# Performance work log

Hardware: AMD Instinct MI355X
Metric: run time of the kernel (lower is better)

Reference implementation:

```python
import jax, jax.numpy as jnp
import numpy as np

BLOCK = 16
H = 16
KV = 4
HPG = H // KV
DH = 64
SCALE = 1.0 / np.sqrt(DH).astype(np.float32)


def setup_inputs() -> dict:
    key = jax.random.key(0)
    ks = jax.random.split(key, 7)
    B, Ldec, Lenc, D = 2, 8192, 4096, 1024
    s = 1.0 / np.sqrt(D).astype(np.float32)
    return {
        "hidden_states": jax.random.normal(ks[0], (B, Ldec, D), jnp.float32),
        "encoder_hidden_states": jax.random.normal(ks[1], (B, Lenc, D), jnp.float32),
        "attention_mask": jax.random.randint(ks[2], (B, Lenc), 0, 2, jnp.int32),
        "Wq": jax.random.normal(ks[3], (D, H * DH), jnp.float32) * s,
        "Wk": jax.random.normal(ks[4], (D, KV * DH), jnp.float32) * s,
        "Wv": jax.random.normal(ks[5], (D, KV * DH), jnp.float32) * s,
        "Wo": jax.random.normal(ks[6], (H * DH, D), jnp.float32) * s,
    }


def reference(hidden_states, encoder_hidden_states, attention_mask, Wq, Wk, Wv, Wo):
    B, Ldec, D = hidden_states.shape
    Lenc = encoder_hidden_states.shape[1]
    pad = (BLOCK - Ldec % BLOCK) % BLOCK
    x = jnp.pad(hidden_states, ((0, 0), (0, pad), (0, 0))) if pad else hidden_states
    nb = (Ldec + pad) // BLOCK
    # mean-pool decoder tokens into blocks: [B, nb, D]
    pooled = x.reshape(B, nb, BLOCK, D).mean(axis=2)
    # projections; GQA: group q heads by kv head (repeat_interleave order)
    q = (pooled @ Wq).reshape(B, nb, KV, HPG, DH)          # [B, nb, KV, HPG, DH]
    k = (encoder_hidden_states @ Wk).reshape(B, Lenc, KV, DH)
    v = (encoder_hidden_states @ Wv).reshape(B, Lenc, KV, DH)
    scores = jnp.einsum("bngqd,blgd->bgqnl", q, k) * SCALE  # [B, KV, HPG, nb, Lenc]
    mask = (attention_mask == 0)[:, None, None, None, :]
    scores = jnp.where(mask, jnp.float32(-1e9), scores)
    attn = jax.nn.softmax(scores, axis=-1)
    out = jnp.einsum("bgqnl,blgd->bngqd", attn, v)          # [B, nb, KV, HPG, DH]
    out = out.reshape(B, nb, H * DH) @ Wo                   # [B, nb, D]
    # broadcast block output back to token level
    unpooled = jnp.broadcast_to(out[:, :, None, :], (B, nb, BLOCK, D)).reshape(B, nb * BLOCK, D)
    return unpooled[:, :Ldec, :]
```

## Files before the change

### kernel.cpp

```cpp
#include <hip/hip_runtime.h>


typedef unsigned short u16;
typedef __attribute__((ext_vector_type(8))) __bf16 bf16x8;
typedef __attribute__((ext_vector_type(4))) float f32x4;
typedef __attribute__((ext_vector_type(4))) _Float16 f16x4;

static __device__ __forceinline__ u16 f2bf(float f) {
    unsigned int u = __float_as_uint(f);
    u = (u + 0x7fffu + ((u >> 16) & 1u)) >> 16;
    return (u16)u;
}
static __device__ __forceinline__ void gload16(const u16* g, u16* l) {
    __builtin_amdgcn_global_load_lds(
        (const __attribute__((address_space(1))) void*)g,
        (__attribute__((address_space(3))) void*)l, 16, 0, 0);
}

__global__ __launch_bounds__(256) void prep_all(const float* __restrict__ enc,
                                                const float* __restrict__ hid,
                                                const int* __restrict__ mask,
                                                const float* __restrict__ Wq,
                                                const float* __restrict__ Wk,
                                                const float* __restrict__ Wv,
                                                const float* __restrict__ Wo,
                                                u16* __restrict__ encb,
                                                u16* __restrict__ poolb,
                                                u16* __restrict__ mh,
                                                u16* __restrict__ Wq_t,
                                                u16* __restrict__ Wkv_t,
                                                u16* __restrict__ Wo_t) {
    int bid = blockIdx.x;
    if (bid < 1024) {
        const int row = bid;
        const int c4 = threadIdx.x;
        const float4* src = (const float4*)(hid + (size_t)row * 16 * 1024) + c4;
        float4 v[16];
#pragma unroll
        for (int t = 0; t < 16; ++t) v[t] = src[(size_t)t * 256];
#pragma unroll
        for (int t = 0; t < 8; ++t) {
            v[t].x += v[t + 8].x; v[t].y += v[t + 8].y;
            v[t].z += v[t + 8].z; v[t].w += v[t + 8].w;
        }
#pragma unroll
        for (int t = 0; t < 4; ++t) {
            v[t].x += v[t + 4].x; v[t].y += v[t + 4].y;
            v[t].z += v[t + 4].z; v[t].w += v[t + 4].w;
        }
#pragma unroll
        for (int t = 0; t < 2; ++t) {
            v[t].x += v[t + 2].x; v[t].y += v[t + 2].y;
            v[t].z += v[t + 2].z; v[t].w += v[t + 2].w;
        }
        v[0].x += v[1].x; v[0].y += v[1].y; v[0].z += v[1].z; v[0].w += v[1].w;
        ushort4 o;
        o.x = f2bf(v[0].x * 0.0625f); o.y = f2bf(v[0].y * 0.0625f);
        o.z = f2bf(v[0].z * 0.0625f); o.w = f2bf(v[0].w * 0.0625f);
        *(ushort4*)(poolb + (size_t)row * 1024 + c4 * 4) = o;
    } else if (bid < 2048) {
        const int base = (bid - 1024) * 2048 + threadIdx.x;
        float4 v[8];
#pragma unroll
        for (int j = 0; j < 8; ++j) v[j] = ((const float4*)enc)[base + j * 256];
#pragma unroll
        for (int j = 0; j < 8; ++j) {
            ushort4 o;
            o.x = f2bf(v[j].x); o.y = f2bf(v[j].y);
            o.z = f2bf(v[j].z); o.w = f2bf(v[j].w);
            ((ushort4*)encb)[base + j * 256] = o;
        }
    } else if (bid < 4608) {
        bid -= 2048;
        const float* in; u16* out; int N, nbx, rowoff;
        if (bid < 1024)      { in = Wq; out = Wq_t;  N = 1024; nbx = 32; rowoff = 0; }
        else if (bid < 2048) { in = Wo; out = Wo_t;  N = 1024; nbx = 32; rowoff = 0; bid -= 1024; }
        else if (bid < 2304) { in = Wk; out = Wkv_t; N = 256;  nbx = 8;  rowoff = 0; bid -= 2048; }
        else                 { in = Wv; out = Wkv_t; N = 256;  nbx = 8;  rowoff = 256; bid -= 2304; }
        const int n0 = (bid % nbx) * 32, k0 = (bid / nbx) * 32;
        __shared__ float t[32][33];
        const int tx = threadIdx.x & 31, ty = threadIdx.x >> 5;
#pragma unroll
        for (int i = 0; i < 4; ++i)
            t[ty + 8 * i][tx] = in[(size_t)(k0 + ty + 8 * i) * N + n0 + tx];
        __syncthreads();
#pragma unroll
        for (int i = 0; i < 4; ++i)
            out[(size_t)(rowoff + n0 + ty + 8 * i) * 1024 + k0 + tx] = f2bf(t[tx][ty + 8 * i]);
    } else {
#pragma unroll
        for (int k = 0; k < 32; ++k) {
            const int i = threadIdx.x + 256 * k;
            mh[i] = mask[i] ? (u16)0x3C00 : (u16)0;
        }
    }
}

template <int MODE>
static __device__ __forceinline__ void gemm_core(const u16* __restrict__ A,
                                                 const u16* __restrict__ Bt,
                                                 u16* __restrict__ outQ,
                                                 float* __restrict__ out_f,
                                                 int m0, int n0, int kt0, int nkt,
                                                 u16* sAB) {
    u16* sA = sAB;
    u16* sB = sAB + 64 * 64;
    const int t = threadIdx.x;
    const int w = t >> 6, lane = t & 63, quad = lane >> 4, r16 = lane & 15;
    const int row8 = lane >> 3, seg = lane & 7;
    const int sseg = ((seg ^ row8) << 3);
    const int rsw = r16 & 7;

    f32x4 acc[4];
#pragma unroll
    for (int i = 0; i < 4; ++i) acc[i] = (f32x4){0.f, 0.f, 0.f, 0.f};

    for (int kt = kt0; kt < kt0 + nkt; ++kt) {
        const int k0 = kt * 64;
        __syncthreads();
#pragma unroll
        for (int j = 0; j < 2; ++j) {
            const int ra = w * 16 + j * 8;
            gload16(A + (size_t)(m0 + ra + row8) * 1024 + k0 + sseg, sA + ra * 64);
            gload16(Bt + (size_t)(n0 + ra + row8) * 1024 + k0 + sseg, sB + ra * 64);
        }
        __syncthreads();
#pragma unroll
        for (int kk = 0; kk < 2; ++kk) {
            const int csw = ((kk * 4 + quad) ^ rsw) << 3;
            const bf16x8 af = *(const bf16x8*)(sA + (16 * w + r16) * 64 + csw);
#pragma unroll
            for (int nt = 0; nt < 4; ++nt) {
                const bf16x8 bfv = *(const bf16x8*)(sB + (nt * 16 + r16) * 64 + csw);
                acc[nt] = __builtin_amdgcn_mfma_f32_16x16x32_bf16(af, bfv, acc[nt], 0, 0, 0);
            }
        }
    }

    if (MODE == 0) {
#pragma unroll
        for (int nt = 0; nt < 4; ++nt)
#pragma unroll
            for (int r = 0; r < 4; ++r) {
                const int m = m0 + 16 * w + quad * 4 + r;
                const int c = n0 + nt * 16 + r16;
                const int b = m >> 9, nq = m & 511, g = c >> 8, qh = (c >> 6) & 3, d = c & 63;
                outQ[((((size_t)(b * 4 + g) * 4 + qh) * 512 + nq) << 6) + d] =
                    f2bf(acc[nt][r] * 0.180336880f);
            }
    } else {
#pragma unroll
        for (int nt = 0; nt < 4; ++nt)
#pragma unroll
            for (int r = 0; r < 4; ++r) {
                const int m = m0 + 16 * w + quad * 4 + r;
                const int c = n0 + nt * 16 + r16;
                out_f[(size_t)m * 1024 + c] = acc[nt][r];
            }
    }
}

__global__ __launch_bounds__(256) void gemm_qkv(const u16* __restrict__ poolb,
                                                const u16* __restrict__ encb,
                                                const u16* __restrict__ Wq_t,
                                                const u16* __restrict__ Wkv_t,
                                                const int* __restrict__ maskp,
                                                u16* __restrict__ Qa,
                                                u16* __restrict__ Ka,
                                                u16* __restrict__ Va) {
    __shared__ __align__(16) u16 smem[12288];
    const int bx = blockIdx.x;
    if (bx >= 512) {
        const int b = bx - 512;
        gemm_core<0>(poolb, Wq_t, Qa, nullptr, (b >> 4) * 64, (b & 15) * 64, 0, 16, smem);
        return;
    }
    const int xcd = bx & 7, j = bx >> 3;
    const int mt = xcd * 8 + (j & 7), nt2 = j >> 3;
    const int m0 = mt * 128, n0 = nt2 * 64;
    u16* sA = smem;
    u16* sB = smem + 128 * 64;
    const int t = threadIdx.x;
    const int w = t >> 6, lane = t & 63, quad = lane >> 4, r16 = lane & 15;
    const int row8 = lane >> 3, seg = lane & 7;
    const int sseg = ((seg ^ row8) << 3);
    const int rsw = r16 & 7;

    f32x4 acc[2][4];
#pragma unroll
    for (int i = 0; i < 2; ++i)
#pragma unroll
        for (int nt = 0; nt < 4; ++nt) acc[i][nt] = (f32x4){0.f, 0.f, 0.f, 0.f};

    for (int kt = 0; kt < 16; ++kt) {
        const int k0 = kt * 64;
        __syncthreads();
#pragma unroll
        for (int p = 0; p < 4; ++p) {
            const int ra = p * 32 + w * 8;
            gload16(encb + (size_t)(m0 + ra + row8) * 1024 + k0 + sseg, sA + ra * 64);
        }
#pragma unroll
        for (int p = 0; p < 2; ++p) {
            const int ra = p * 32 + w * 8;
            gload16(Wkv_t + (size_t)(n0 + ra + row8) * 1024 + k0 + sseg, sB + ra * 64);
        }
        __syncthreads();
#pragma unroll
        for (int kk = 0; kk < 2; ++kk) {
            const int csw = ((kk * 4 + quad) ^ rsw) << 3;
#pragma unroll
            for (int i = 0; i < 2; ++i) {
                const bf16x8 af = *(const bf16x8*)(sA + (w * 32 + i * 16 + r16) * 64 + csw);
#pragma unroll
                for (int nt = 0; nt < 4; ++nt) {
                    const bf16x8 bfv = *(const bf16x8*)(sB + (nt * 16 + r16) * 64 + csw);
                    acc[i][nt] = __builtin_amdgcn_mfma_f32_16x16x32_bf16(af, bfv, acc[i][nt], 0, 0, 0);
                }
            }
        }
    }

    const bool isV = (n0 >= 256);
    const int g = (isV ? (n0 - 256) : n0) >> 6;
    const int b = m0 >> 12, l0 = m0 & 4095;
    __syncthreads();
    if (isV) {
        u16* sT = smem;
#pragma unroll
        for (int i = 0; i < 2; ++i) {
            float mfl[4];
#pragma unroll
            for (int r = 0; r < 4; ++r)
                mfl[r] = maskp[b * 4096 + l0 + w * 32 + i * 16 + quad * 4 + r] ? 1.f : 0.f;
#pragma unroll
            for (int nt = 0; nt < 4; ++nt)
#pragma unroll
                for (int r = 0; r < 4; ++r) {
                    const int ml = w * 32 + i * 16 + quad * 4 + r, cl = nt * 16 + r16;
                    union { _Float16 h; u16 u; } cv;
                    cv.h = (_Float16)(acc[i][nt][r] * mfl[r]);
                    sT[cl * 136 + ml] = cv.u;
                }
        }
        __syncthreads();
#pragma unroll
        for (int p = 0; p < 4; ++p) {
            const int idx = t + 256 * p, rr = idx >> 4, ch = idx & 15;
            *(int4*)(Va + ((size_t)(b * 4 + g) * 64 + rr) * 4096 + l0 + ch * 8) =
                *(const int4*)(sT + rr * 136 + ch * 8);
        }
    } else {
        u16* sT = smem;
#pragma unroll
        for (int i = 0; i < 2; ++i)
#pragma unroll
            for (int nt = 0; nt < 4; ++nt)
#pragma unroll
                for (int r = 0; r < 4; ++r) {
                    const int ml = w * 32 + i * 16 + quad * 4 + r, cl = nt * 16 + r16;
                    sT[ml * 72 + cl] = f2bf(acc[i][nt][r]);
                }
        __syncthreads();
#pragma unroll
        for (int p = 0; p < 4; ++p) {
            const int idx = t + 256 * p, rr = idx >> 3, ch = idx & 7;
            *(int4*)(Ka + (((size_t)(b * 4 + g) * 4096 + l0 + rr) << 6) + ch * 8) =
                *(const int4*)(sT + rr * 72 + ch * 8);
        }
    }
}

__global__ __launch_bounds__(256) void gemm_o_bcast(const u16* __restrict__ attn,
                                                    const u16* __restrict__ Wo_t,
                                                    float* __restrict__ out) {
    __shared__ __align__(16) u16 smem[2][4096];
    const int bx = blockIdx.x;
    const int m0 = (bx >> 5) * 32, n0 = (bx & 31) * 32;
    const int t = threadIdx.x;
    const int w = t >> 6, lane = t & 63, quad = lane >> 4, r16 = lane & 15;
    const int row8 = lane >> 3, seg = lane & 7;
    const int sseg = ((seg ^ row8) << 3);
    const int rsw = r16 & 7;
    const int wr = w >> 1, wc = w & 1;

    f32x4 acc = (f32x4){0.f, 0.f, 0.f, 0.f};

    auto stage = [&](int kt, int bi) {
        const int k0 = kt * 64;
        u16* sA = smem[bi];
        u16* sB = smem[bi] + 2048;
        gload16(attn + (size_t)(m0 + w * 8 + row8) * 1024 + k0 + sseg, sA + w * 8 * 64);
        gload16(Wo_t + (size_t)(n0 + w * 8 + row8) * 1024 + k0 + sseg, sB + w * 8 * 64);
    };
    stage(0, 0);
    for (int kt = 0; kt < 16; ++kt) {
        const int bi = kt & 1;
        __syncthreads();
        if (kt < 15) stage(kt + 1, bi ^ 1);
        const u16* sA = smem[bi];
        const u16* sB = smem[bi] + 2048;
#pragma unroll
        for (int kk = 0; kk < 2; ++kk) {
            const int csw = ((kk * 4 + quad) ^ rsw) << 3;
            const bf16x8 af = *(const bf16x8*)(sA + (wr * 16 + r16) * 64 + csw);
            const bf16x8 bfv = *(const bf16x8*)(sB + (wc * 16 + r16) * 64 + csw);
            acc = __builtin_amdgcn_mfma_f32_16x16x32_bf16(af, bfv, acc, 0, 0, 0);
        }
    }
    __syncthreads();
    float* sf = (float*)smem;
#pragma unroll
    for (int r = 0; r < 4; ++r)
        sf[(wr * 16 + quad * 4 + r) * 36 + wc * 16 + r16] = acc[r];
    __syncthreads();
    const int row = t >> 3, ch = t & 7;
    const f32x4 v = *(const f32x4*)(sf + row * 36 + ch * 4);
    const int m = m0 + row, b = m >> 9, n = m & 511;
    f32x4* dst = (f32x4*)(out + ((size_t)b * 8192 + (size_t)n * 16) * 1024 + n0) + ch;
#pragma unroll
    for (int rep = 0; rep < 16; ++rep)
        __builtin_nontemporal_store(v, dst + (size_t)rep * 256);
}

__global__ __launch_bounds__(1024, 4) void flash_attn(const u16* __restrict__ Qa,
                                                      const u16* __restrict__ Ka,
                                                      const u16* __restrict__ Vt,
                                                      const u16* __restrict__ mh,
                                                      u16* __restrict__ attnout) {
    const int bx = blockIdx.x;
    const int gb = bx & 7, s16 = bx >> 3;
    const int g = gb & 3, b = gb >> 2;
    __shared__ __align__(16) u16 sKV[4][2][4096];
    const int t = threadIdx.x;
    const int wv = t >> 6, grp = wv >> 2, qh = wv & 3;
    const int lane = t & 63, quad = lane >> 4, r16 = lane & 15;

    u16* sK = sKV[grp][0];
    u16* sV = sKV[grp][1];

    bf16x8 aq[2];
    {
        const size_t qbase = ((((size_t)gb * 4 + qh) * 512) + s16 * 16 + r16) * 64;
#pragma unroll
        for (int kk = 0; kk < 2; ++kk)
            aq[kk] = *(const bf16x8*)(Qa + qbase + kk * 32 + quad * 8);
    }
    const u16* Kg = Ka + (size_t)gb * 4096 * 64;
    const u16* Vg = Vt + (size_t)gb * 64 * 4096;
    const u16* mb = mh + b * 4096 + quad * 4;

    const int tg = t & 255;
    const int r0 = tg >> 3, ks = tg & 7, r1 = r0 + 32;
    const int off0 = (r0 * 64 + ks * 8) ^ ((r0 & 7) << 3);
    const int off1 = (r1 * 64 + ks * 8) ^ ((r1 & 7) << 3);

    f32x4 o[4], lacc;
#pragma unroll
    for (int i = 0; i < 4; ++i) o[i] = (f32x4){0.f, 0.f, 0.f, 0.f};
    lacc = (f32x4){0.f, 0.f, 0.f, 0.f};

    int4 rk0, rk1, rv0, rv1;
    auto ldtile = [&](int l0) {
        rk0 = *(const int4*)(Kg + (size_t)(l0 + r0) * 64 + ks * 8);
        rk1 = *(const int4*)(Kg + (size_t)(l0 + r1) * 64 + ks * 8);
        rv0 = *(const int4*)(Vg + (size_t)r0 * 4096 + l0 + ks * 8);
        rv1 = *(const int4*)(Vg + (size_t)r1 * 4096 + l0 + ks * 8);
    };
    auto sttile = [&]() {
        *(int4*)(sK + off0) = rk0;
        *(int4*)(sK + off1) = rk1;
        *(int4*)(sV + off0) = rv0;
        *(int4*)(sV + off1) = rv1;
    };

    ldtile(grp * 64);
    for (int i = 0; i < 16; ++i) {
        const int l0 = (i * 4 + grp) * 64;
        sttile();
        __syncthreads();
        if (i < 15) ldtile(l0 + 256);

        f32x4 st[4];
#pragma unroll
        for (int nt = 0; nt < 4; ++nt) st[nt] = (f32x4){0.f, 0.f, 0.f, 0.f};
#pragma unroll
        for (int kk = 0; kk < 2; ++kk)
#pragma unroll
            for (int nt = 0; nt < 4; ++nt) {
                const int kidx = ((nt * 16 + r16) * 64 + kk * 32 + quad * 8) ^ ((r16 & 7) << 3);
                const bf16x8 ka = *(const bf16x8*)(sK + kidx);
                st[nt] = __builtin_amdgcn_mfma_f32_16x16x32_bf16(ka, aq[kk], st[nt], 0, 0, 0);
            }

#pragma unroll
        for (int nt = 0; nt < 4; ++nt) {
            f16x4 pa;
#pragma unroll
            for (int j = 0; j < 4; ++j)
                pa[j] = (_Float16)__builtin_amdgcn_exp2f(st[nt][j]);
            const f16x4 bvm = *(const f16x4*)(mb + l0 + nt * 16);
            lacc = __builtin_amdgcn_mfma_f32_16x16x16f16(pa, bvm, lacc, 0, 0, 0);
#pragma unroll
            for (int dt = 0; dt < 4; ++dt) {
                const int vidx = ((dt * 16 + r16) * 64 + nt * 16 + quad * 4) ^ ((r16 & 7) << 3);
                const f16x4 bv = *(const f16x4*)(sV + vidx);
                o[dt] = __builtin_amdgcn_mfma_f32_16x16x16f16(pa, bv, o[dt], 0, 0, 0);
            }
        }
        __syncthreads();
    }

    float* fp = (float*)sKV;
    if (grp > 0) {
#pragma unroll
        for (int dt = 0; dt < 4; ++dt)
#pragma unroll
            for (int r = 0; r < 4; ++r)
                fp[(grp - 1) * 4096 + qh * 1024 + (quad * 4 + r) * 64 + dt * 16 + r16] = o[dt][r];
        if (r16 == 0) {
#pragma unroll
            for (int r = 0; r < 4; ++r)
                fp[12288 + ((grp - 1) * 4 + qh) * 16 + quad * 4 + r] = lacc[r];
        }
    }
    __syncthreads();
    if (grp == 0) {
        float Ls[4];
#pragma unroll
        for (int r = 0; r < 4; ++r) Ls[r] = lacc[r];
#pragma unroll
        for (int p = 0; p < 3; ++p) {
#pragma unroll
            for (int dt = 0; dt < 4; ++dt)
#pragma unroll
                for (int r = 0; r < 4; ++r)
                    o[dt][r] += fp[p * 4096 + qh * 1024 + (quad * 4 + r) * 64 + dt * 16 + r16];
#pragma unroll
            for (int r = 0; r < 4; ++r)
                Ls[r] += fp[12288 + (p * 4 + qh) * 16 + quad * 4 + r];
        }
        const size_t obase = ((size_t)b * 512 + s16 * 16) * 1024 + (g * 4 + qh) * 64;
#pragma unroll
        for (int r = 0; r < 4; ++r) {
            const float invL = 1.f / Ls[r];
            const size_t rbase = obase + (size_t)(quad * 4 + r) * 1024;
#pragma unroll
            for (int dt = 0; dt < 4; ++dt)
                attnout[rbase + dt * 16 + r16] = f2bf(o[dt][r] * invL);
        }
    }
}

extern "C" void kernel_launch(void* const* d_in, const int* in_sizes, int n_in,
                              void* d_out, int out_size, void* d_ws, size_t ws_size,
                              hipStream_t stream) {
    const float* hid  = (const float*)d_in[0];
    const float* enc  = (const float*)d_in[1];
    const int*   mask = (const int*)d_in[2];
    const float* Wq   = (const float*)d_in[3];
    const float* Wk   = (const float*)d_in[4];
    const float* Wv   = (const float*)d_in[5];
    const float* Wo   = (const float*)d_in[6];
    float* out = (float*)d_out;

    char* ws = (char*)d_ws;
    size_t off = 0;
    auto alloc = [&](size_t bytes) -> char* {
        char* p = ws + off;
        off += (bytes + 255) & ~(size_t)255;
        return p;
    };
    u16* Wq_t  = (u16*)alloc((size_t)1024 * 1024 * 2);
    u16* Wkv_t = (u16*)alloc((size_t)512 * 1024 * 2);
    u16* Wo_t  = (u16*)alloc((size_t)1024 * 1024 * 2);
    u16* encb  = (u16*)alloc((size_t)8192 * 1024 * 2);
    u16* poolb = (u16*)alloc((size_t)1024 * 1024 * 2);
    u16* Qa    = (u16*)alloc((size_t)1024 * 1024 * 2);
    u16* Ka    = (u16*)alloc((size_t)8 * 4096 * 64 * 2);
    u16* Va    = (u16*)alloc((size_t)8 * 4096 * 64 * 2);
    u16* attn  = (u16*)alloc((size_t)1024 * 1024 * 2);
    u16* mh    = (u16*)alloc((size_t)8192 * 2);

    prep_all<<<4609, 256, 0, stream>>>(enc, hid, mask, Wq, Wk, Wv, Wo,
                                       encb, poolb, mh, Wq_t, Wkv_t, Wo_t);
    gemm_qkv<<<768, 256, 0, stream>>>(poolb, encb, Wq_t, Wkv_t, mask, Qa, Ka, Va);
    flash_attn<<<256, 1024, 0, stream>>>(Qa, Ka, Va, mh, attn);
    gemm_o_bcast<<<1024, 256, 0, stream>>>(attn, Wo_t, out);
}
```

Baseline: 220.0 us.

## Shrink KV projection tiles to 64x64 via shared gemm core and force load batching

The KV projection GEMM now uses 64x64 tiles through the shared gemm_core instead of 128x64 tiles. This doubles the block count from 512 to 1024 for better occupancy and CU balance, at the cost of reloading the weight tiles more often. gemm_core now returns its accumulators to the caller, so the K/V epilogue is resized to match. Empty asm barriers in the prep kernel force all global loads to be issued before any arithmetic so more loads are in flight.

```diff
diff --git a/kernel.cpp b/kernel.cpp
--- a/kernel.cpp
+++ b/kernel.cpp
@@ -38,6 +38,11 @@
         float4 v[16];
 #pragma unroll
         for (int t = 0; t < 16; ++t) v[t] = src[(size_t)t * 256];
+        asm volatile("" ::
+            "v"(v[0].x),  "v"(v[1].x),  "v"(v[2].x),  "v"(v[3].x),
+            "v"(v[4].x),  "v"(v[5].x),  "v"(v[6].x),  "v"(v[7].x),
+            "v"(v[8].x),  "v"(v[9].x),  "v"(v[10].x), "v"(v[11].x),
+            "v"(v[12].x), "v"(v[13].x), "v"(v[14].x), "v"(v[15].x));
 #pragma unroll
         for (int t = 0; t < 8; ++t) {
             v[t].x += v[t + 8].x; v[t].y += v[t + 8].y;
@@ -63,6 +68,9 @@
         float4 v[8];
 #pragma unroll
         for (int j = 0; j < 8; ++j) v[j] = ((const float4*)enc)[base + j * 256];
+        asm volatile("" ::
+            "v"(v[0].x), "v"(v[1].x), "v"(v[2].x), "v"(v[3].x),
+            "v"(v[4].x), "v"(v[5].x), "v"(v[6].x), "v"(v[7].x));
 #pragma unroll
         for (int j = 0; j < 8; ++j) {
             ushort4 o;
@@ -100,7 +108,7 @@
 static __device__ __forceinline__ void gemm_core(const u16* __restrict__ A,
                                                  const u16* __restrict__ Bt,
                                                  u16* __restrict__ outQ,
-                                                 float* __restrict__ out_f,
+                                                 f32x4* accout,
                                                  int m0, int n0, int kt0, int nkt,
                                                  u16* sAB) {
     u16* sA = sAB;
@@ -150,13 +158,7 @@
             }
     } else {
 #pragma unroll
-        for (int nt = 0; nt < 4; ++nt)
-#pragma unroll
-            for (int r = 0; r < 4; ++r) {
-                const int m = m0 + 16 * w + quad * 4 + r;
-                const int c = n0 + nt * 16 + r16;
-                out_f[(size_t)m * 1024 + c] = acc[nt][r];
-            }
+        for (int nt = 0; nt < 4; ++nt) accout[nt] = acc[nt];
     }
 }
 
@@ -168,102 +170,60 @@
                                                 u16* __restrict__ Qa,
                                                 u16* __restrict__ Ka,
                                                 u16* __restrict__ Va) {
-    __shared__ __align__(16) u16 smem[12288];
+    __shared__ __align__(16) u16 smem[8192];
     const int bx = blockIdx.x;
-    if (bx >= 512) {
-        const int b = bx - 512;
+    if (bx >= 1024) {
+        const int b = bx - 1024;
         gemm_core<0>(poolb, Wq_t, Qa, nullptr, (b >> 4) * 64, (b & 15) * 64, 0, 16, smem);
         return;
     }
     const int xcd = bx & 7, j = bx >> 3;
-    const int mt = xcd * 8 + (j & 7), nt2 = j >> 3;
-    const int m0 = mt * 128, n0 = nt2 * 64;
-    u16* sA = smem;
-    u16* sB = smem + 128 * 64;
+    const int mt = xcd * 16 + (j & 15), nt2 = j >> 4;
+    const int m0 = mt * 64, n0 = nt2 * 64;
+
+    f32x4 acc[4];
+    gemm_core<1>(encb, Wkv_t, nullptr, acc, m0, n0, 0, 16, smem);
+
     const int t = threadIdx.x;
     const int w = t >> 6, lane = t & 63, quad = lane >> 4, r16 = lane & 15;
-    const int row8 = lane >> 3, seg = lane & 7;
-    const int sseg = ((seg ^ row8) << 3);
-    const int rsw = r16 & 7;
-
-    f32x4 acc[2][4];
-#pragma unroll
-    for (int i = 0; i < 2; ++i)
-#pragma unroll
-        for (int nt = 0; nt < 4; ++nt) acc[i][nt] = (f32x4){0.f, 0.f, 0.f, 0.f};
-
-    for (int kt = 0; kt < 16; ++kt) {
-        const int k0 = kt * 64;
-        __syncthreads();
-#pragma unroll
-        for (int p = 0; p < 4; ++p) {
-            const int ra = p * 32 + w * 8;
-            gload16(encb + (size_t)(m0 + ra + row8) * 1024 + k0 + sseg, sA + ra * 64);
-        }
-#pragma unroll
-        for (int p = 0; p < 2; ++p) {
-            const int ra = p * 32 + w * 8;
-            gload16(Wkv_t + (size_t)(n0 + ra + row8) * 1024 + k0 + sseg, sB + ra * 64);
-        }
-        __syncthreads();
-#pragma unroll
-        for (int kk = 0; kk < 2; ++kk) {
-            const int csw = ((kk * 4 + quad) ^ rsw) << 3;
-#pragma unroll
-            for (int i = 0; i < 2; ++i) {
-                const bf16x8 af = *(const bf16x8*)(sA + (w * 32 + i * 16 + r16) * 64 + csw);
-#pragma unroll
-                for (int nt = 0; nt < 4; ++nt) {
-                    const bf16x8 bfv = *(const bf16x8*)(sB + (nt * 16 + r16) * 64 + csw);
-                    acc[i][nt] = __builtin_amdgcn_mfma_f32_16x16x32_bf16(af, bfv, acc[i][nt], 0, 0, 0);
-                }
-            }
-        }
-    }
-
     const bool isV = (n0 >= 256);
     const int g = (isV ? (n0 - 256) : n0) >> 6;
     const int b = m0 >> 12, l0 = m0 & 4095;
     __syncthreads();
     if (isV) {
         u16* sT = smem;
-#pragma unroll
-        for (int i = 0; i < 2; ++i) {
-            float mfl[4];
-#pragma unroll
-            for (int r = 0; r < 4; ++r)
-                mfl[r] = maskp[b * 4096 + l0 + w * 32 + i * 16 + quad * 4 + r] ? 1.f : 0.f;
-#pragma unroll
-            for (int nt = 0; nt < 4; ++nt)
-#pragma unroll
-                for (int r = 0; r < 4; ++r) {
-                    const int ml = w * 32 + i * 16 + quad * 4 + r, cl = nt * 16 + r16;
-                    union { _Float16 h; u16 u; } cv;
-                    cv.h = (_Float16)(acc[i][nt][r] * mfl[r]);
-                    sT[cl * 136 + ml] = cv.u;
-                }
-        }
-        __syncthreads();
-#pragma unroll
-        for (int p = 0; p < 4; ++p) {
-            const int idx = t + 256 * p, rr = idx >> 4, ch = idx & 15;
+        float mfl[4];
+#pragma unroll
+        for (int r = 0; r < 4; ++r)
+            mfl[r] = maskp[b * 4096 + l0 + w * 16 + quad * 4 + r] ? 1.f : 0.f;
+#pragma unroll
+        for (int nt = 0; nt < 4; ++nt)
+#pragma unroll
+            for (int r = 0; r < 4; ++r) {
+                const int ml = w * 16 + quad * 4 + r, cl = nt * 16 + r16;
+                union { _Float16 h; u16 u; } cv;
+                cv.h = (_Float16)(acc[nt][r] * mfl[r]);
+                sT[cl * 72 + ml] = cv.u;
+            }
+        __syncthreads();
+#pragma unroll
+        for (int p = 0; p < 2; ++p) {
+            const int idx = t + 256 * p, rr = idx >> 3, ch = idx & 7;
             *(int4*)(Va + ((size_t)(b * 4 + g) * 64 + rr) * 4096 + l0 + ch * 8) =
-                *(const int4*)(sT + rr * 136 + ch * 8);
+                *(const int4*)(sT + rr * 72 + ch * 8);
         }
     } else {
         u16* sT = smem;
 #pragma unroll
-        for (int i = 0; i < 2; ++i)
-#pragma unroll
-            for (int nt = 0; nt < 4; ++nt)
-#pragma unroll
-                for (int r = 0; r < 4; ++r) {
-                    const int ml = w * 32 + i * 16 + quad * 4 + r, cl = nt * 16 + r16;
-                    sT[ml * 72 + cl] = f2bf(acc[i][nt][r]);
-                }
-        __syncthreads();
-#pragma unroll
-        for (int p = 0; p < 4; ++p) {
+        for (int nt = 0; nt < 4; ++nt)
+#pragma unroll
+            for (int r = 0; r < 4; ++r) {
+                const int ml = w * 16 + quad * 4 + r, cl = nt * 16 + r16;
+                sT[ml * 72 + cl] = f2bf(acc[nt][r]);
+            }
+        __syncthreads();
+#pragma unroll
+        for (int p = 0; p < 2; ++p) {
             const int idx = t + 256 * p, rr = idx >> 3, ch = idx & 7;
             *(int4*)(Ka + (((size_t)(b * 4 + g) * 4096 + l0 + rr) << 6) + ch * 8) =
                 *(const int4*)(sT + rr * 72 + ch * 8);
@@ -484,7 +444,7 @@
 
     prep_all<<<4609, 256, 0, stream>>>(enc, hid, mask, Wq, Wk, Wv, Wo,
                                        encb, poolb, mh, Wq_t, Wkv_t, Wo_t);
-    gemm_qkv<<<768, 256, 0, stream>>>(poolb, encb, Wq_t, Wkv_t, mask, Qa, Ka, Va);
+    gemm_qkv<<<1280, 256, 0, stream>>>(poolb, encb, Wq_t, Wkv_t, mask, Qa, Ka, Va);
     flash_attn<<<256, 1024, 0, stream>>>(Qa, Ka, Va, mh, attn);
     gemm_o_bcast<<<1024, 256, 0, stream>>>(attn, Wo_t, out);
 }
```

Result: no change. 223.5 us (+1.6%).
